# Kernel optimization log

Hardware: AMD Instinct MI355X
Metric: run time of the kernel (lower is better)

Reference implementation:

```python
import jax, jax.numpy as jnp
import numpy as np
import math

EMSIZE = 256
NHEAD = 8
HEAD = EMSIZE // NHEAD
SEQ = 2048
BATCH = 2


def setup_inputs() -> dict:
    key = jax.random.key(0)
    ks = jax.random.split(key, 8)
    s = 1.0 / math.sqrt(EMSIZE)
    return {
        "em": jax.random.normal(ks[0], (SEQ, BATCH, EMSIZE), jnp.float32),
        "mask": jnp.zeros((BATCH, 1, SEQ, SEQ), jnp.float32),
        "Wq": jax.random.normal(ks[1], (EMSIZE, EMSIZE), jnp.float32) * s,
        "bq": jnp.zeros((EMSIZE,), jnp.float32),
        "Wk": jax.random.normal(ks[2], (EMSIZE, EMSIZE), jnp.float32) * s,
        "bk": jnp.zeros((EMSIZE,), jnp.float32),
        "Wv": jax.random.normal(ks[3], (EMSIZE, EMSIZE), jnp.float32) * s,
        "bv": jnp.zeros((EMSIZE,), jnp.float32),
    }


def reference(em, mask, Wq, bq, Wk, bk, Wv, bv):
    # em: [S, B, E] -> [B, S, E]
    x = jnp.swapaxes(em, 0, 1)
    B, S, E = x.shape
    H, D = NHEAD, HEAD
    # QKV projections (nn.Linear: x @ W.T + b), split heads -> [B, S, H, D]
    q = (x @ Wq.T + bq).reshape(B, S, H, D)
    k = (x @ Wk.T + bk).reshape(B, S, H, D)
    v = (x @ Wv.T + bv).reshape(B, S, H, D)
    # scores: [B, H, S, S]
    scores = jnp.einsum("bqhd,bkhd->bhqk", q, k) / math.sqrt(D) + mask
    attn = jax.nn.softmax(scores, axis=-1)  # dropout in eval mode = identity
    # context: [B, S, H, D] -> [B, S, E] -> [S, B, E]
    ctx = jnp.einsum("bhqk,bkhd->bqhd", attn, v).reshape(B, S, E)
    return jnp.swapaxes(ctx, 0, 1)
```

## Files before the change

### kernel.cpp

```cpp
#include <hip/hip_runtime.h>
#include <hip/hip_bf16.h>

typedef float f32x4 __attribute__((ext_vector_type(4)));
typedef float f32x16 __attribute__((ext_vector_type(16)));
typedef __bf16 bf16x8 __attribute__((ext_vector_type(8)));
typedef int v2i __attribute__((ext_vector_type(2)));
typedef unsigned short ushort_t;

#define SEQ 2048
#define BATCH 2
#define EMS 256
#define NHEAD 8
#define HEAD 32
#define BH (BATCH*NHEAD)
#define LOG2E 1.4426950408889634f
#define QSCALE 0.2550348211f
#define THRS 11.5415603f

static __device__ __forceinline__ ushort_t f2bfbits(float f) {
    unsigned int u = __float_as_uint(f);
    u += 0x7fffu + ((u >> 16) & 1u);
    return (ushort_t)(u >> 16);
}

static __device__ __forceinline__ unsigned cvtpk(float lo, float hi) {
    unsigned r;
    asm("v_cvt_pk_bf16_f32 %0, %1, %2" : "=v"(r) : "v"(lo), "v"(hi));
    return r;
}

static __device__ __forceinline__ float exp2a(float x) {
    float r;
    asm("v_exp_f32 %0, %1" : "=v"(r) : "v"(x));
    return r;
}

static __device__ __forceinline__ bf16x8 cvt8(const float* p) {
    float4 a = *reinterpret_cast<const float4*>(p);
    float4 b = *reinterpret_cast<const float4*>(p + 4);
    union { bf16x8 v; uint4 u; } x;
    x.u.x = cvtpk(a.x, a.y);
    x.u.y = cvtpk(a.z, a.w);
    x.u.z = cvtpk(b.x, b.y);
    x.u.w = cvtpk(b.z, b.w);
    return x.v;
}

__global__ __launch_bounds__(256) void qkv_proj(
    const float* __restrict__ em,
    const float* __restrict__ Wq, const float* __restrict__ bq,
    const float* __restrict__ Wk, const float* __restrict__ bk,
    const float* __restrict__ Wv, const float* __restrict__ bv,
    ushort_t* __restrict__ Qb, ushort_t* __restrict__ Kb,
    ushort_t* __restrict__ Vb)
{
    int wid = blockIdx.x * 4 + (threadIdx.x >> 6);
    int l   = threadIdx.x & 63;
    int l15 = l & 15, lq = l >> 4;
    int rb = wid / 12, cg = wid % 12;
    int r0 = rb * 32, c0 = cg * 64;
    int sel = c0 >> 8;
    const float* W    = sel == 0 ? Wq : (sel == 1 ? Wk : Wv);
    const float* bias = sel == 0 ? bq : (sel == 1 ? bk : bv);
    ushort_t*    dst  = sel == 0 ? Qb : (sel == 1 ? Kb : Vb);
    int cb = c0 & 255;

    f32x4 acc[2][4];
    #pragma unroll
    for (int m = 0; m < 2; m++)
        #pragma unroll
        for (int n = 0; n < 4; n++) acc[m][n] = (f32x4){0.f, 0.f, 0.f, 0.f};

    #pragma unroll
    for (int kk = 0; kk < 8; kk++) {
        int k0 = kk * 32;
        bf16x8 af[2], bfm[4];
        #pragma unroll
        for (int m = 0; m < 2; m++)
            af[m] = cvt8(em + (size_t)(r0 + m * 16 + l15) * EMS + k0 + lq * 8);
        #pragma unroll
        for (int n = 0; n < 4; n++)
            bfm[n] = cvt8(W + (size_t)(cb + n * 16 + l15) * EMS + k0 + lq * 8);
        #pragma unroll
        for (int m = 0; m < 2; m++)
            #pragma unroll
            for (int n = 0; n < 4; n++)
                acc[m][n] = __builtin_amdgcn_mfma_f32_16x16x32_bf16(af[m], bfm[n], acc[m][n], 0, 0, 0);
    }

    float scale = (sel == 0) ? QSCALE : 1.0f;
    #pragma unroll
    for (int m = 0; m < 2; m++) {
        #pragma unroll
        for (int n = 0; n < 4; n++) {
            int c = cb + n * 16 + l15;
            float bv_ = bias[c];
            int h = c >> 5, d = c & 31;
            #pragma unroll
            for (int r = 0; r < 4; r++) {
                int row = r0 + m * 16 + lq * 4 + r;
                int s = row >> 1, b = row & 1;
                ushort_t v = f2bfbits((acc[m][n][r] + bv_) * scale);
                dst[((size_t)(b * NHEAD + h) * SEQ + s) * HEAD + d] = v;
            }
        }
    }
}

__global__ __launch_bounds__(256) void vtrans(const ushort_t* __restrict__ Vb,
                                              ushort_t* __restrict__ Vt2)
{
    __shared__ ushort_t t[64][40];
    int g = blockIdx.x;
    int bh = g & 15, st = g >> 4;
    int s0 = st * 64;
    int tid = threadIdx.x;

    {
        int sl = tid >> 2, d0 = (tid & 3) * 8;
        uint4 v = *(const uint4*)(Vb + ((size_t)bh * SEQ + s0 + sl) * HEAD + d0);
        *(uint4*)&t[sl][d0] = v;
    }
    __syncthreads();
    {
        int kb_l = tid >> 7, rem = tid & 127;
        int d = rem >> 2, si0 = (rem & 3) * 8;
        union { ushort_t u[8]; uint4 q; } o;
        #pragma unroll
        for (int j = 0; j < 8; j++) o.u[j] = t[kb_l * 32 + si0 + j][d];
        *(uint4*)(Vt2 + (((size_t)bh * 64 + (s0 >> 5) + kb_l) * 32 + d) * 32 + si0) = o.q;
    }
}

__global__ __launch_bounds__(256, 2) void mask_scan(
    const float* __restrict__ mask, unsigned* __restrict__ flagsG)
{
    int sb = blockIdx.x;
    int kh = sb & 1, qt = (sb >> 1) & 127, b = sb >> 8;
    int t = threadIdx.x;
    const float* base = mask + ((size_t)b * SEQ + qt * 16) * SEQ + kh * 1024 + t * 4;
    float4 v[16];
    #pragma unroll
    for (int it = 0; it < 16; it++)
        v[it] = *(const float4*)(base + (size_t)it * SEQ);
    unsigned acc = 0;
    #pragma unroll
    for (int it = 0; it < 16; it++)
        acc |= __float_as_uint(v[it].x) | __float_as_uint(v[it].y)
             | __float_as_uint(v[it].z) | __float_as_uint(v[it].w);
    unsigned nz = (acc & 0x7fffffffu) != 0u;

    __shared__ unsigned fl;
    if (t == 0) fl = 0;
    __syncthreads();
    if (nz) atomicOr(&fl, 1u << (t >> 3));
    __syncthreads();
    if (t == 0) flagsG[(b * 128 + qt) * 2 + kh] = fl;
}

__global__ __launch_bounds__(256, 4) void attn(
    const ushort_t* __restrict__ Qb, const ushort_t* __restrict__ Kb,
    const ushort_t* __restrict__ Vt2, const float* __restrict__ mask,
    const unsigned long long* __restrict__ flagsG, float* __restrict__ out)
{
    int g  = blockIdx.x;
    int qt = g >> 4;
    int b  = (g >> 3) & 1;
    int h  = g & 7;
    int bh = b * NHEAD + h;
    int w  = threadIdx.x >> 6;
    int l  = threadIdx.x & 63;
    int l31 = l & 31, hi = l >> 5;
    int qs0 = qt * 32;

    __shared__ float oacc[4][32][36];
    __shared__ float om[4][32], ol[4][32];

    const ushort_t* qrow = Qb + ((size_t)bh * SEQ + qs0 + l31) * HEAD + hi * 8;
    bf16x8 qf0 = *(const bf16x8*)(qrow);
    bf16x8 qf1 = *(const bf16x8*)(qrow + 16);

    unsigned long long fbits = flagsG[b * 128 + qt * 2] | flagsG[b * 128 + qt * 2 + 1];

    f32x16 acc = {};
    float mrun = -1e30f, lsum = 0.f;

    int k0 = w * (SEQ / 4);
    const ushort_t* kbase = Kb  + ((size_t)bh * SEQ + k0 + l31) * HEAD + hi * 8;
    const ushort_t* vbase = Vt2 + ((size_t)bh * 64 + (k0 >> 5)) * 1024 + l31 * 32 + hi * 8;

    bf16x8 kc0 = *(const bf16x8*)(kbase);
    bf16x8 kc1 = *(const bf16x8*)(kbase + 16);
    bf16x8 vc0 = *(const bf16x8*)(vbase);
    bf16x8 vc1 = *(const bf16x8*)(vbase + 16);

    const int NT = (SEQ / 4) / 32;
    for (int kt = 0; kt < NT; kt++) {
        int ktn = (kt + 1 < NT) ? kt + 1 : 0;
        f32x16 st = {};
        st = __builtin_amdgcn_mfma_f32_32x32x16_bf16(kc0, qf0, st, 0, 0, 0);
        st = __builtin_amdgcn_mfma_f32_32x32x16_bf16(kc1, qf1, st, 0, 0, 0);

        bf16x8 kn0 = *(const bf16x8*)(kbase + ktn * 1024);
        bf16x8 kn1 = *(const bf16x8*)(kbase + ktn * 1024 + 16);
        bf16x8 vn0 = *(const bf16x8*)(vbase + ktn * 1024);
        bf16x8 vn1 = *(const bf16x8*)(vbase + ktn * 1024 + 16);

        if ((fbits >> (w * 16 + kt)) & 1ull) {
            const float* mr = mask + (size_t)b * SEQ * SEQ
                            + (size_t)(qs0 + l31) * SEQ + k0 + kt * 32 + hi * 4;
            union { float4 f4[4]; float f[16]; } mu;
            mu.f4[0] = *(const float4*)(mr);
            mu.f4[1] = *(const float4*)(mr + 8);
            mu.f4[2] = *(const float4*)(mr + 16);
            mu.f4[3] = *(const float4*)(mr + 24);
            #pragma unroll
            for (int j = 0; j < 16; j++) st[j] += mu.f[j] * LOG2E;
        }

        float x0 = fmaxf(st[0], st[1]),  x1 = fmaxf(st[2], st[3]);
        float x2 = fmaxf(st[4], st[5]),  x3 = fmaxf(st[6], st[7]);
        float x4 = fmaxf(st[8], st[9]),  x5 = fmaxf(st[10], st[11]);
        float x6 = fmaxf(st[12], st[13]), x7 = fmaxf(st[14], st[15]);
        float lmax = fmaxf(fmaxf(fmaxf(x0, x1), fmaxf(x2, x3)),
                           fmaxf(fmaxf(x4, x5), fmaxf(x6, x7)));

        if (__any(lmax > mrun + THRS)) {
            v2i sw = __builtin_amdgcn_permlane32_swap(
                __float_as_int(lmax), __float_as_int(lmax), false, false);
            float pm = fmaxf(fmaxf(lmax, __int_as_float(sw.x)), __int_as_float(sw.y));
            float nm = fmaxf(mrun, pm);
            float sc = exp2a(mrun - nm);
            lsum *= sc;
            #pragma unroll
            for (int j = 0; j < 16; j++) acc[j] *= sc;
            mrun = nm;
        }

        float ev[16];
        #pragma unroll
        for (int j = 0; j < 16; j++) ev[j] = exp2a(st[j] - mrun);
        lsum += (((ev[0]+ev[1])+(ev[2]+ev[3])) + ((ev[4]+ev[5])+(ev[6]+ev[7])))
              + (((ev[8]+ev[9])+(ev[10]+ev[11])) + ((ev[12]+ev[13])+(ev[14]+ev[15])));

        unsigned pk[8];
        #pragma unroll
        for (int j = 0; j < 8; j++) pk[j] = cvtpk(ev[2 * j], ev[2 * j + 1]);
        v2i p0 = __builtin_amdgcn_permlane32_swap((int)pk[0], (int)pk[2], false, false);
        v2i p1 = __builtin_amdgcn_permlane32_swap((int)pk[1], (int)pk[3], false, false);
        v2i p2 = __builtin_amdgcn_permlane32_swap((int)pk[4], (int)pk[6], false, false);
        v2i p3 = __builtin_amdgcn_permlane32_swap((int)pk[5], (int)pk[7], false, false);
        union { int i[4]; bf16x8 v; } pf0, pf1;
        pf0.i[0] = p0.x; pf0.i[1] = p1.x; pf0.i[2] = p0.y; pf0.i[3] = p1.y;
        pf1.i[0] = p2.x; pf1.i[1] = p3.x; pf1.i[2] = p2.y; pf1.i[3] = p3.y;

        acc = __builtin_amdgcn_mfma_f32_32x32x16_bf16(vc0, pf0.v, acc, 0, 0, 0);
        acc = __builtin_amdgcn_mfma_f32_32x32x16_bf16(vc1, pf1.v, acc, 0, 0, 0);

        kc0 = kn0; kc1 = kn1; vc0 = vn0; vc1 = vn1;
    }

    v2i sl = __builtin_amdgcn_permlane32_swap(
        __float_as_int(lsum), __float_as_int(lsum), false, false);
    float lt = __int_as_float(sl.x) + __int_as_float(sl.y);
    if (hi == 0) { om[w][l31] = mrun; ol[w][l31] = lt; }

    #pragma unroll
    for (int gg = 0; gg < 4; gg++) {
        f32x4 vv = { acc[4*gg], acc[4*gg+1], acc[4*gg+2], acc[4*gg+3] };
        *(f32x4*)&oacc[w][l31][8 * gg + 4 * hi] = vv;
    }
    __syncthreads();

    int t = threadIdx.x;
    int q = t >> 3, d4 = (t & 7) * 4;
    float m0 = om[0][q], m1 = om[1][q], m2 = om[2][q], m3 = om[3][q];
    float mg = fmaxf(fmaxf(m0, m1), fmaxf(m2, m3));
    float w0_ = exp2a(m0 - mg), w1_ = exp2a(m1 - mg);
    float w2_ = exp2a(m2 - mg), w3_ = exp2a(m3 - mg);
    float lg = w0_ * ol[0][q] + w1_ * ol[1][q] + w2_ * ol[2][q] + w3_ * ol[3][q];
    float inv = 1.0f / lg;
    float4 o;
    o.x = (w0_*oacc[0][q][d4]   + w1_*oacc[1][q][d4]   + w2_*oacc[2][q][d4]   + w3_*oacc[3][q][d4])   * inv;
    o.y = (w0_*oacc[0][q][d4+1] + w1_*oacc[1][q][d4+1] + w2_*oacc[2][q][d4+1] + w3_*oacc[3][q][d4+1]) * inv;
    o.z = (w0_*oacc[0][q][d4+2] + w1_*oacc[1][q][d4+2] + w2_*oacc[2][q][d4+2] + w3_*oacc[3][q][d4+2]) * inv;
    o.w = (w0_*oacc[0][q][d4+3] + w1_*oacc[1][q][d4+3] + w2_*oacc[2][q][d4+3] + w3_*oacc[3][q][d4+3]) * inv;
    *(float4*)(out + ((size_t)(qs0 + q) * BATCH + b) * EMS + h * HEAD + d4) = o;
}

extern "C" void kernel_launch(void* const* d_in, const int* in_sizes, int n_in,
                              void* d_out, int out_size, void* d_ws, size_t ws_size,
                              hipStream_t stream) {
    const float* em  = (const float*)d_in[0];
    const float* mask = (const float*)d_in[1];
    const float* Wq  = (const float*)d_in[2];
    const float* bq  = (const float*)d_in[3];
    const float* Wk  = (const float*)d_in[4];
    const float* bk  = (const float*)d_in[5];
    const float* Wv  = (const float*)d_in[6];
    const float* bv  = (const float*)d_in[7];
    float* out = (float*)d_out;

    ushort_t* Qb  = (ushort_t*)d_ws;
    ushort_t* Kb  = Qb + (size_t)BH * SEQ * HEAD;
    ushort_t* Vb  = Kb + (size_t)BH * SEQ * HEAD;
    ushort_t* Vt2 = Vb + (size_t)BH * SEQ * HEAD;
    unsigned* flagsG = (unsigned*)(Vt2 + (size_t)BH * SEQ * HEAD);

    qkv_proj<<<dim3(384), dim3(256), 0, stream>>>(em, Wq, bq, Wk, bk, Wv, bv, Qb, Kb, Vb);
    vtrans<<<dim3(512), dim3(256), 0, stream>>>(Vb, Vt2);
    mask_scan<<<dim3(512), dim3(256), 0, stream>>>(mask, flagsG);
    attn<<<dim3(1024), dim3(256), 0, stream>>>(Qb, Kb, Vt2, mask,
                                               (const unsigned long long*)flagsG, out);
}
```

Baseline: 57.18 us.

## Drop mask-scan kernel; always prefetch mask tiles in attention and reorder blocks

Removes the separate mask_scan launch and its per-tile nonzero flags. The attention loop now always reads the mask tile, double-buffered alongside the K/V prefetch, and adds it with fma. The block index is remapped to head-major order, so consecutive blocks share (h, b) instead of sharing a query tile across heads. This saves one kernel launch and the scan pass, but the attention kernel now reads the full fp32 mask for every head. The new block order also reduces L2 reuse of mask rows across heads, so mask traffic rises sharply.

```diff
diff --git a/kernel.cpp b/kernel.cpp
--- a/kernel.cpp
+++ b/kernel.cpp
@@ -132,41 +132,16 @@
     }
 }
 
-__global__ __launch_bounds__(256, 2) void mask_scan(
-    const float* __restrict__ mask, unsigned* __restrict__ flagsG)
-{
-    int sb = blockIdx.x;
-    int kh = sb & 1, qt = (sb >> 1) & 127, b = sb >> 8;
-    int t = threadIdx.x;
-    const float* base = mask + ((size_t)b * SEQ + qt * 16) * SEQ + kh * 1024 + t * 4;
-    float4 v[16];
-    #pragma unroll
-    for (int it = 0; it < 16; it++)
-        v[it] = *(const float4*)(base + (size_t)it * SEQ);
-    unsigned acc = 0;
-    #pragma unroll
-    for (int it = 0; it < 16; it++)
-        acc |= __float_as_uint(v[it].x) | __float_as_uint(v[it].y)
-             | __float_as_uint(v[it].z) | __float_as_uint(v[it].w);
-    unsigned nz = (acc & 0x7fffffffu) != 0u;
-
-    __shared__ unsigned fl;
-    if (t == 0) fl = 0;
-    __syncthreads();
-    if (nz) atomicOr(&fl, 1u << (t >> 3));
-    __syncthreads();
-    if (t == 0) flagsG[(b * 128 + qt) * 2 + kh] = fl;
-}
-
 __global__ __launch_bounds__(256, 4) void attn(
     const ushort_t* __restrict__ Qb, const ushort_t* __restrict__ Kb,
     const ushort_t* __restrict__ Vt2, const float* __restrict__ mask,
-    const unsigned long long* __restrict__ flagsG, float* __restrict__ out)
+    float* __restrict__ out)
 {
-    int g  = blockIdx.x;
-    int qt = g >> 4;
-    int b  = (g >> 3) & 1;
-    int h  = g & 7;
+    int g   = blockIdx.x;
+    int h   = g >> 7;
+    int rem = g & 127;
+    int b   = rem >> 6;
+    int qt  = rem & 63;
     int bh = b * NHEAD + h;
     int w  = threadIdx.x >> 6;
     int l  = threadIdx.x & 63;
@@ -180,19 +155,23 @@
     bf16x8 qf0 = *(const bf16x8*)(qrow);
     bf16x8 qf1 = *(const bf16x8*)(qrow + 16);
 
-    unsigned long long fbits = flagsG[b * 128 + qt * 2] | flagsG[b * 128 + qt * 2 + 1];
-
     f32x16 acc = {};
     float mrun = -1e30f, lsum = 0.f;
 
     int k0 = w * (SEQ / 4);
     const ushort_t* kbase = Kb  + ((size_t)bh * SEQ + k0 + l31) * HEAD + hi * 8;
     const ushort_t* vbase = Vt2 + ((size_t)bh * 64 + (k0 >> 5)) * 1024 + l31 * 32 + hi * 8;
+    const float*    mbase = mask + (size_t)b * SEQ * SEQ
+                          + (size_t)(qs0 + l31) * SEQ + k0 + hi * 4;
 
     bf16x8 kc0 = *(const bf16x8*)(kbase);
     bf16x8 kc1 = *(const bf16x8*)(kbase + 16);
     bf16x8 vc0 = *(const bf16x8*)(vbase);
     bf16x8 vc1 = *(const bf16x8*)(vbase + 16);
+    float4 mc0 = *(const float4*)(mbase);
+    float4 mc1 = *(const float4*)(mbase + 8);
+    float4 mc2 = *(const float4*)(mbase + 16);
+    float4 mc3 = *(const float4*)(mbase + 24);
 
     const int NT = (SEQ / 4) / 32;
     for (int kt = 0; kt < NT; kt++) {
@@ -205,18 +184,20 @@
         bf16x8 kn1 = *(const bf16x8*)(kbase + ktn * 1024 + 16);
         bf16x8 vn0 = *(const bf16x8*)(vbase + ktn * 1024);
         bf16x8 vn1 = *(const bf16x8*)(vbase + ktn * 1024 + 16);
-
-        if ((fbits >> (w * 16 + kt)) & 1ull) {
-            const float* mr = mask + (size_t)b * SEQ * SEQ
-                            + (size_t)(qs0 + l31) * SEQ + k0 + kt * 32 + hi * 4;
-            union { float4 f4[4]; float f[16]; } mu;
-            mu.f4[0] = *(const float4*)(mr);
-            mu.f4[1] = *(const float4*)(mr + 8);
-            mu.f4[2] = *(const float4*)(mr + 16);
-            mu.f4[3] = *(const float4*)(mr + 24);
-            #pragma unroll
-            for (int j = 0; j < 16; j++) st[j] += mu.f[j] * LOG2E;
-        }
+        const float* mrn = mbase + ktn * 32;
+        float4 mn0 = *(const float4*)(mrn);
+        float4 mn1 = *(const float4*)(mrn + 8);
+        float4 mn2 = *(const float4*)(mrn + 16);
+        float4 mn3 = *(const float4*)(mrn + 24);
+
+        st[0]  = fmaf(mc0.x, LOG2E, st[0]);  st[1]  = fmaf(mc0.y, LOG2E, st[1]);
+        st[2]  = fmaf(mc0.z, LOG2E, st[2]);  st[3]  = fmaf(mc0.w, LOG2E, st[3]);
+        st[4]  = fmaf(mc1.x, LOG2E, st[4]);  st[5]  = fmaf(mc1.y, LOG2E, st[5]);
+        st[6]  = fmaf(mc1.z, LOG2E, st[6]);  st[7]  = fmaf(mc1.w, LOG2E, st[7]);
+        st[8]  = fmaf(mc2.x, LOG2E, st[8]);  st[9]  = fmaf(mc2.y, LOG2E, st[9]);
+        st[10] = fmaf(mc2.z, LOG2E, st[10]); st[11] = fmaf(mc2.w, LOG2E, st[11]);
+        st[12] = fmaf(mc3.x, LOG2E, st[12]); st[13] = fmaf(mc3.y, LOG2E, st[13]);
+        st[14] = fmaf(mc3.z, LOG2E, st[14]); st[15] = fmaf(mc3.w, LOG2E, st[15]);
 
         float x0 = fmaxf(st[0], st[1]),  x1 = fmaxf(st[2], st[3]);
         float x2 = fmaxf(st[4], st[5]),  x3 = fmaxf(st[6], st[7]);
@@ -258,6 +239,7 @@
         acc = __builtin_amdgcn_mfma_f32_32x32x16_bf16(vc1, pf1.v, acc, 0, 0, 0);
 
         kc0 = kn0; kc1 = kn1; vc0 = vn0; vc1 = vn1;
+        mc0 = mn0; mc1 = mn1; mc2 = mn2; mc3 = mn3;
     }
 
     v2i sl = __builtin_amdgcn_permlane32_swap(
@@ -305,11 +287,8 @@
     ushort_t* Kb  = Qb + (size_t)BH * SEQ * HEAD;
     ushort_t* Vb  = Kb + (size_t)BH * SEQ * HEAD;
     ushort_t* Vt2 = Vb + (size_t)BH * SEQ * HEAD;
-    unsigned* flagsG = (unsigned*)(Vt2 + (size_t)BH * SEQ * HEAD);
 
     qkv_proj<<<dim3(384), dim3(256), 0, stream>>>(em, Wq, bq, Wk, bk, Wv, bv, Qb, Kb, Vb);
     vtrans<<<dim3(512), dim3(256), 0, stream>>>(Vb, Vt2);
-    mask_scan<<<dim3(512), dim3(256), 0, stream>>>(mask, flagsG);
-    attn<<<dim3(1024), dim3(256), 0, stream>>>(Qb, Kb, Vt2, mask,
-                                               (const unsigned long long*)flagsG, out);
-}
+    attn<<<dim3(1024), dim3(256), 0, stream>>>(Qb, Kb, Vt2, mask, out);
+}
```

Result: slower. 77.75 us (+36.0%).

## Fuse mask scan into QKV projection kernel with atomic flag bitmap

Applied to the files above, without the earlier changes.

Merges the separate mask-scan kernel into the QKV projection launch: the first 2048 blocks stream the 32 MB mask with nontemporal loads and atomically OR per-tile nonzero bits into a flag bitmap, and the remaining blocks run the projection. A memset clears the flags beforehand, and the mask add in attention becomes an FMA. This removes one kernel launch and lets the mask read overlap with the projection work. In exchange it adds a memset launch and global atomics whenever mask tiles are nonzero.

```diff
diff --git a/kernel.cpp b/kernel.cpp
--- a/kernel.cpp
+++ b/kernel.cpp
@@ -5,6 +5,7 @@
 typedef float f32x16 __attribute__((ext_vector_type(16)));
 typedef __bf16 bf16x8 __attribute__((ext_vector_type(8)));
 typedef int v2i __attribute__((ext_vector_type(2)));
+typedef unsigned int u32x4 __attribute__((ext_vector_type(4)));
 typedef unsigned short ushort_t;
 
 #define SEQ 2048
@@ -46,15 +47,41 @@
     return x.v;
 }
 
-__global__ __launch_bounds__(256) void qkv_proj(
-    const float* __restrict__ em,
+__global__ __launch_bounds__(256) void fused_pre(
+    const float* __restrict__ em, const float* __restrict__ mask,
     const float* __restrict__ Wq, const float* __restrict__ bq,
     const float* __restrict__ Wk, const float* __restrict__ bk,
     const float* __restrict__ Wv, const float* __restrict__ bv,
     ushort_t* __restrict__ Qb, ushort_t* __restrict__ Kb,
-    ushort_t* __restrict__ Vb)
+    ushort_t* __restrict__ Vb, unsigned* __restrict__ flagsU)
 {
-    int wid = blockIdx.x * 4 + (threadIdx.x >> 6);
+    if (blockIdx.x < 2048) {
+        int tid = blockIdx.x * 256 + threadIdx.x;
+        const u32x4* m4 = (const u32x4*)mask;
+        unsigned nz[4];
+        int idx[4];
+        #pragma unroll
+        for (int i = 0; i < 4; i++) {
+            int o = tid + i * 524288;
+            u32x4 v = __builtin_nontemporal_load(&m4[o]);
+            nz[i] = ((v.x | v.y | v.z | v.w) << 1);
+            idx[i] = o;
+        }
+        #pragma unroll
+        for (int i = 0; i < 4; i++) {
+            if (nz[i]) {
+                int o = idx[i];
+                int row = o >> 9;
+                int b = row >> 11, q = row & 2047;
+                int kt = (o & 511) >> 3;
+                int us = (b * 128 + (q >> 4)) * 4 + (kt >> 4);
+                atomicOr(flagsU + (us >> 1), (1u << (kt & 15)) << ((us & 1) * 16));
+            }
+        }
+        return;
+    }
+
+    int wid = (blockIdx.x - 2048) * 4 + (threadIdx.x >> 6);
     int l   = threadIdx.x & 63;
     int l15 = l & 15, lq = l >> 4;
     int rb = wid / 12, cg = wid % 12;
@@ -130,32 +157,6 @@
         for (int j = 0; j < 8; j++) o.u[j] = t[kb_l * 32 + si0 + j][d];
         *(uint4*)(Vt2 + (((size_t)bh * 64 + (s0 >> 5) + kb_l) * 32 + d) * 32 + si0) = o.q;
     }
-}
-
-__global__ __launch_bounds__(256, 2) void mask_scan(
-    const float* __restrict__ mask, unsigned* __restrict__ flagsG)
-{
-    int sb = blockIdx.x;
-    int kh = sb & 1, qt = (sb >> 1) & 127, b = sb >> 8;
-    int t = threadIdx.x;
-    const float* base = mask + ((size_t)b * SEQ + qt * 16) * SEQ + kh * 1024 + t * 4;
-    float4 v[16];
-    #pragma unroll
-    for (int it = 0; it < 16; it++)
-        v[it] = *(const float4*)(base + (size_t)it * SEQ);
-    unsigned acc = 0;
-    #pragma unroll
-    for (int it = 0; it < 16; it++)
-        acc |= __float_as_uint(v[it].x) | __float_as_uint(v[it].y)
-             | __float_as_uint(v[it].z) | __float_as_uint(v[it].w);
-    unsigned nz = (acc & 0x7fffffffu) != 0u;
-
-    __shared__ unsigned fl;
-    if (t == 0) fl = 0;
-    __syncthreads();
-    if (nz) atomicOr(&fl, 1u << (t >> 3));
-    __syncthreads();
-    if (t == 0) flagsG[(b * 128 + qt) * 2 + kh] = fl;
 }
 
 __global__ __launch_bounds__(256, 4) void attn(
@@ -215,7 +216,7 @@
             mu.f4[2] = *(const float4*)(mr + 16);
             mu.f4[3] = *(const float4*)(mr + 24);
             #pragma unroll
-            for (int j = 0; j < 16; j++) st[j] += mu.f[j] * LOG2E;
+            for (int j = 0; j < 16; j++) st[j] = fmaf(mu.f[j], LOG2E, st[j]);
         }
 
         float x0 = fmaxf(st[0], st[1]),  x1 = fmaxf(st[2], st[3]);
@@ -305,11 +306,12 @@
     ushort_t* Kb  = Qb + (size_t)BH * SEQ * HEAD;
     ushort_t* Vb  = Kb + (size_t)BH * SEQ * HEAD;
     ushort_t* Vt2 = Vb + (size_t)BH * SEQ * HEAD;
-    unsigned* flagsG = (unsigned*)(Vt2 + (size_t)BH * SEQ * HEAD);
-
-    qkv_proj<<<dim3(384), dim3(256), 0, stream>>>(em, Wq, bq, Wk, bk, Wv, bv, Qb, Kb, Vb);
+    unsigned* flagsU = (unsigned*)(Vt2 + (size_t)BH * SEQ * HEAD);
+
+    (void)hipMemsetAsync(flagsU, 0, 2048, stream);
+    fused_pre<<<dim3(2432), dim3(256), 0, stream>>>(em, mask, Wq, bq, Wk, bk, Wv, bv,
+                                                    Qb, Kb, Vb, flagsU);
     vtrans<<<dim3(512), dim3(256), 0, stream>>>(Vb, Vt2);
-    mask_scan<<<dim3(512), dim3(256), 0, stream>>>(mask, flagsG);
     attn<<<dim3(1024), dim3(256), 0, stream>>>(Qb, Kb, Vt2, mask,
-                                               (const unsigned long long*)flagsG, out);
-}
+                                               (const unsigned long long*)flagsU, out);
+}
```

New measurement: 69.93 us. +22.3%, slower.
